# Performance work log

Hardware: AMD Instinct MI355X
Metric: run time of the kernel (lower is better)

## Reference

```python
import jax, jax.numpy as jnp
import numpy as np

NUM_USERS = 100000
NUM_ITEMS = 50000
NUM_NODES = NUM_USERS + NUM_ITEMS
EMBED_DIM = 64
NUM_LAYERS = 3
NUM_EDGES = 1200000


def setup_inputs() -> dict:
    key = jax.random.key(0)
    k1, k2 = jax.random.split(key)
    edge_index = jax.random.randint(k1, (2, NUM_EDGES), 0, NUM_NODES, dtype=jnp.int32)
    # xavier_uniform for [N, D]
    limit = float(np.sqrt(6.0 / (NUM_NODES + EMBED_DIM)))
    embedding = jax.random.uniform(k2, (NUM_NODES, EMBED_DIM), dtype=jnp.float32,
                                   minval=-limit, maxval=limit)
    return {"edge_index": edge_index, "embedding": embedding}


def reference(edge_index, embedding):
    n = embedding.shape[0]
    row, col = edge_index[0], edge_index[1]
    ones = jnp.ones((edge_index.shape[1],), dtype=embedding.dtype)
    deg_row = jax.ops.segment_sum(ones, row, num_segments=n)
    deg_col = jax.ops.segment_sum(ones, col, num_segments=n)
    # deg^-0.5 with inf (deg==0) -> 0
    inv_row = jnp.where(deg_row > 0, jax.lax.rsqrt(jnp.maximum(deg_row, 1e-30)), 0.0)
    inv_col = jnp.where(deg_col > 0, jax.lax.rsqrt(jnp.maximum(deg_col, 1e-30)), 0.0)
    norm = (inv_row[row] * inv_col[col])[:, None]  # [E, 1]

    x = embedding
    accum = x
    for _ in range(NUM_LAYERS):
        # gather source embeddings, scale by symmetric norm, scatter-add at target
        msgs = norm * x[row]                       # [E, D]
        x = jax.ops.segment_sum(msgs, col, num_segments=n)
        accum = accum + x
    final = accum / jnp.asarray(NUM_LAYERS + 1, dtype=embedding.dtype)
    return final[:NUM_USERS], final[NUM_USERS:]
```

## Files before the change

### kernel.cpp

```cpp
#include <hip/hip_runtime.h>
#include <hip/hip_fp16.h>


constexpr int NUM_USERS = 100000;
constexpr int NUM_ITEMS = 50000;
constexpr int N_NODES   = NUM_USERS + NUM_ITEMS;
constexpr int EMBED_DIM = 64;
constexpr int NUM_EDGES = 1200000;
constexpr int SHIFT = 9;
constexpr int BSZ   = 1 << SHIFT;
constexpr int NBUCK = (N_NODES + BSZ - 1) >> SHIFT;
constexpr int CAPC  = 4480;
constexpr int EPB   = 4096;
constexpr int P1_BLOCKS = (NUM_EDGES + EPB - 1) / EPB;

__global__ void __launch_bounds__(256)
pass1_bin(const int4* __restrict__ row4, const int4* __restrict__ col4,
          int* __restrict__ gcur_c, int* __restrict__ gcur_r,
          unsigned int* __restrict__ binned_c, unsigned short* __restrict__ binned_r) {
    __shared__ int hist_c[NBUCK], hist_r[NBUCK], cur_c[NBUCK], cur_r[NBUCK];
    int t = threadIdx.x;
    for (int i = t; i < NBUCK; i += 256) { hist_c[i] = 0; hist_r[i] = 0; }
    __syncthreads();
    int base4 = blockIdx.x * (EPB / 4);
    constexpr int NV = NUM_EDGES / 4;
    for (int k = 0; k < EPB / 1024; ++k) {
        int v = base4 + k * 256 + t;
        if (v < NV) {
            int4 c = col4[v];
            atomicAdd(&hist_c[c.x >> SHIFT], 1);
            atomicAdd(&hist_c[c.y >> SHIFT], 1);
            atomicAdd(&hist_c[c.z >> SHIFT], 1);
            atomicAdd(&hist_c[c.w >> SHIFT], 1);
            int4 r = row4[v];
            atomicAdd(&hist_r[r.x >> SHIFT], 1);
            atomicAdd(&hist_r[r.y >> SHIFT], 1);
            atomicAdd(&hist_r[r.z >> SHIFT], 1);
            atomicAdd(&hist_r[r.w >> SHIFT], 1);
        }
    }
    __syncthreads();
    for (int i = t; i < NBUCK; i += 256) {
        cur_c[i] = atomicAdd(&gcur_c[i], hist_c[i]);
        cur_r[i] = atomicAdd(&gcur_r[i], hist_r[i]);
    }
    __syncthreads();
    for (int k = 0; k < EPB / 1024; ++k) {
        int v = base4 + k * 256 + t;
        if (v < NV) {
            int4 c = col4[v];
            int4 r = row4[v];
            int cc[4] = {c.x, c.y, c.z, c.w};
            int rr[4] = {r.x, r.y, r.z, r.w};
#pragma unroll
            for (int q = 0; q < 4; ++q) {
                int dc = cc[q] >> SHIFT;
                int sc = atomicAdd(&cur_c[dc], 1);
                if (sc < CAPC)
                    binned_c[dc * CAPC + sc] =
                        ((unsigned)(cc[q] & (BSZ - 1)) << 18) | (unsigned)rr[q];
                int dr = rr[q] >> SHIFT;
                int sr = atomicAdd(&cur_r[dr], 1);
                if (sr < CAPC)
                    binned_r[dr * CAPC + sr] = (unsigned short)(rr[q] & (BSZ - 1));
            }
        }
    }
}

__global__ void __launch_bounds__(256)
pass2_place(const int* __restrict__ gcur_c, const int* __restrict__ gcur_r,
            const unsigned int* __restrict__ binned_c, const unsigned short* __restrict__ binned_r,
            int* __restrict__ sorted_idx, int* __restrict__ packed_pc,
            float* __restrict__ inv_col, float* __restrict__ inv_row) {
    __shared__ int hist[BSZ];
    __shared__ int partial[256];
    int t = threadIdx.x;
    hist[t] = 0; hist[t + 256] = 0;
    __syncthreads();
    int b = blockIdx.x;
    if (b < NBUCK) {
        int n = gcur_c[b]; if (n > CAPC) n = CAPC;
        const unsigned int* src = binned_c + b * CAPC;
        for (int i = t; i < n; i += 256) atomicAdd(&hist[src[i] >> 18], 1);
        int s = 0;
        for (int i = t; i < b; i += 256) s += gcur_c[i];
        partial[t] = s;
        __syncthreads();
        for (int off = 128; off > 0; off >>= 1) {
            if (t < off) partial[t] += partial[t + off];
            __syncthreads();
        }
        int bucket_base = partial[0];
        __syncthreads();
        int v0 = hist[t * 2], v1 = hist[t * 2 + 1];
        int sum = v0 + v1;
        partial[t] = sum; __syncthreads();
        for (int off = 1; off < 256; off <<= 1) {
            int tv = (t >= off) ? partial[t - off] : 0;
            __syncthreads();
            partial[t] += tv;
            __syncthreads();
        }
        int excl = partial[t] - sum;
        int o0 = excl, o1 = excl + v0;
        hist[t * 2] = o0; hist[t * 2 + 1] = o1;
        int c0 = (b << SHIFT) | (t * 2);
        if (c0 < N_NODES) {
            packed_pc[c0] = ((bucket_base + o0) << 7) | v0;
            inv_col[c0] = (v0 > 0) ? rsqrtf((float)v0) : 0.0f;
        }
        int c1 = c0 + 1;
        if (c1 < N_NODES) {
            packed_pc[c1] = ((bucket_base + o1) << 7) | v1;
            inv_col[c1] = (v1 > 0) ? rsqrtf((float)v1) : 0.0f;
        }
        __syncthreads();
        for (int i = t; i < n; i += 256) {
            unsigned int w = src[i];
            int lc = w >> 18;
            int r  = (int)(w & 0x3FFFFu);
            int slot = atomicAdd(&hist[lc], 1);
            sorted_idx[bucket_base + slot] = r;
        }
    } else {
        int bb = b - NBUCK;
        int n = gcur_r[bb]; if (n > CAPC) n = CAPC;
        const unsigned short* src = binned_r + bb * CAPC;
        for (int i = t; i < n; i += 256) atomicAdd(&hist[src[i]], 1);
        __syncthreads();
        int c0 = (bb << SHIFT) | (t * 2);
        int v0 = hist[t * 2], v1 = hist[t * 2 + 1];
        if (c0 < N_NODES)     inv_row[c0] = (v0 > 0) ? rsqrtf((float)v0) : 0.0f;
        if (c0 + 1 < N_NODES) inv_row[c0 + 1] = (v1 > 0) ? rsqrtf((float)v1) : 0.0f;
    }
}

__global__ void init_y_kernel(const float* __restrict__ inv_row,
                              const float2* __restrict__ emb2, __half2* __restrict__ y0) {
    int i = blockIdx.x * blockDim.x + threadIdx.x;
    if (i < N_NODES * (EMBED_DIM / 2)) {
        float w = inv_row[i >> 5];
        float2 e = emb2[i];
        y0[i] = __floats2half2_rn(w * e.x, w * e.y);
    }
}

__global__ void __launch_bounds__(256, 8)
layer_kernel(const int* __restrict__ packed_pc,
             const int* __restrict__ sorted_idx,
             const float* __restrict__ inv_row,
             const float* __restrict__ inv_col,
             const __half2* __restrict__ y_src,
             __half2* __restrict__ y_dst,
             float2* __restrict__ out2,
             const float2* __restrict__ emb2,
             int mode) {
    int wid  = (blockIdx.x * blockDim.x + threadIdx.x) >> 6;
    int lane = threadIdx.x & 63;
    if (wid >= N_NODES) return;
    int d2 = lane & 31;
    int eh = lane >> 5;
    int packed = packed_pc[wid];
    int cnt = packed & 127;
    int ptr = packed >> 7;
    int lidx = (cnt > 0) ? (ptr + ((lane < cnt) ? lane : 0)) : 0;
    int idx = sorted_idx[lidx];

    float ax0 = 0.0f, ay0 = 0.0f, ax1 = 0.0f, ay1 = 0.0f;
    int j = 0;
    for (; j + 4 <= cnt; j += 4) {
        int sA = __shfl(idx, j + eh);
        int sB = __shfl(idx, j + 2 + eh);
        float2 vA = __half22float2(y_src[sA * 32 + d2]);
        float2 vB = __half22float2(y_src[sB * 32 + d2]);
        ax0 += vA.x; ay0 += vA.y;
        ax1 += vB.x; ay1 += vB.y;
    }
    for (; j < cnt; j += 2) {
        int jj = j + eh;
        int sA = __shfl(idx, (jj < cnt) ? jj : 0);
        float2 vA = __half22float2(y_src[sA * 32 + d2]);
        if (jj < cnt) { ax0 += vA.x; ay0 += vA.y; }
    }
    float sx = ax0 + ax1;
    float sy = ay0 + ay1;
    sx += __shfl_xor(sx, 32);
    sy += __shfl_xor(sy, 32);

    float invc = inv_col[wid];
    float vx = sx * invc, vy = sy * invc;

    if (lane < 32) {
        int oi2 = wid * 32 + d2;
        if (mode == 0) {
            float w = inv_row[wid];
            y_dst[oi2] = __floats2half2_rn(w * vx, w * vy);
            float2 e = emb2[oi2];
            out2[oi2] = make_float2(e.x + vx, e.y + vy);
        } else if (mode == 1) {
            float w = inv_row[wid];
            y_dst[oi2] = __floats2half2_rn(w * vx, w * vy);
            float2 o = out2[oi2];
            out2[oi2] = make_float2(o.x + vx, o.y + vy);
        } else {
            float2 o = out2[oi2];
            out2[oi2] = make_float2((o.x + vx) * 0.25f, (o.y + vy) * 0.25f);
        }
    }
}

extern "C" void kernel_launch(void* const* d_in, const int* in_sizes, int n_in,
                              void* d_out, int out_size, void* d_ws, size_t ws_size,
                              hipStream_t stream) {
    const int*   edge_index = (const int*)d_in[0];
    const float* embedding  = (const float*)d_in[1];
    const int* row = edge_index;
    const int* col = edge_index + NUM_EDGES;
    float* out = (float*)d_out;

    char* ws = (char*)d_ws;
    auto align_up = [](size_t v) { return (v + 255) & ~size_t(255); };
    size_t off = 0;
    int* gcur_c     = (int*)(ws + off); off = align_up(off + sizeof(int) * NBUCK);
    int* gcur_r     = (int*)(ws + off); off = align_up(off + sizeof(int) * NBUCK);
    size_t cursor_bytes = off;
    int* packed_pc  = (int*)(ws + off); off = align_up(off + sizeof(int) * N_NODES);
    float* inv_row  = (float*)(ws + off); off = align_up(off + sizeof(float) * N_NODES);
    float* inv_col  = (float*)(ws + off); off = align_up(off + sizeof(float) * N_NODES);
    int* sorted_idx = (int*)(ws + off); off = align_up(off + sizeof(int) * NUM_EDGES);
    __half2* ya     = (__half2*)(ws + off); off = align_up(off + sizeof(__half2) * N_NODES * 32);
    __half2* yb     = (__half2*)(ws + off); off = align_up(off + sizeof(__half2) * N_NODES * 32);
    unsigned int*   binned_c = (unsigned int*)yb;
    unsigned short* binned_r = (unsigned short*)((char*)yb + align_up(sizeof(unsigned int) * NBUCK * CAPC));

    hipMemsetAsync(gcur_c, 0, cursor_bytes, stream);
    pass1_bin<<<P1_BLOCKS, 256, 0, stream>>>((const int4*)row, (const int4*)col,
                                             gcur_c, gcur_r, binned_c, binned_r);
    pass2_place<<<2 * NBUCK, 256, 0, stream>>>(gcur_c, gcur_r, binned_c, binned_r,
                                               sorted_idx, packed_pc, inv_col, inv_row);
    {
        int n2 = N_NODES * 32;
        int threads = 256, blocks = (n2 + threads - 1) / threads;
        init_y_kernel<<<blocks, threads, 0, stream>>>(inv_row, (const float2*)embedding, ya);
    }
    {
        int threads = 256;
        int blocks = (N_NODES * 64 + threads - 1) / threads;
        layer_kernel<<<blocks, threads, 0, stream>>>(packed_pc, sorted_idx, inv_row, inv_col,
                                                     ya, yb, (float2*)out,
                                                     (const float2*)embedding, 0);
        layer_kernel<<<blocks, threads, 0, stream>>>(packed_pc, sorted_idx, inv_row, inv_col,
                                                     yb, ya, (float2*)out,
                                                     (const float2*)embedding, 1);
        layer_kernel<<<blocks, threads, 0, stream>>>(packed_pc, sorted_idx, inv_row, inv_col,
                                                     ya, yb , (float2*)out,
                                                     (const float2*)embedding, 2);
    }
}
```

Baseline: 309.9 us.

## Gather eight neighbor rows per wave with 16-byte loads and split epilogue lanes

The layer kernel now has each wave cover eight edges at once, with 8 lanes each reading a 16-byte int4 slice of a half-precision row, instead of two edges with 4-byte loads. Partial sums are combined with three xor shuffles, and the epilogue is split so one lane group writes the half output and another prefetches and updates the float accumulator with float4 accesses. Pass1 binning also uses four times more blocks with one int4 per thread, for more parallelism. The change trades more shuffle reduction work and extra registers for fewer, wider memory transactions and better latency hiding on the random gathers.

```diff
diff --git a/kernel.cpp b/kernel.cpp
--- a/kernel.cpp
+++ b/kernel.cpp
@@ -11,7 +11,7 @@
 constexpr int BSZ   = 1 << SHIFT;
 constexpr int NBUCK = (N_NODES + BSZ - 1) >> SHIFT;
 constexpr int CAPC  = 4480;
-constexpr int EPB   = 4096;
+constexpr int EPB   = 1024;
 constexpr int P1_BLOCKS = (NUM_EDGES + EPB - 1) / EPB;
 
 __global__ void __launch_bounds__(256)
@@ -24,8 +24,8 @@
     __syncthreads();
     int base4 = blockIdx.x * (EPB / 4);
     constexpr int NV = NUM_EDGES / 4;
-    for (int k = 0; k < EPB / 1024; ++k) {
-        int v = base4 + k * 256 + t;
+    {
+        int v = base4 + t;
         if (v < NV) {
             int4 c = col4[v];
             atomicAdd(&hist_c[c.x >> SHIFT], 1);
@@ -45,8 +45,8 @@
         cur_r[i] = atomicAdd(&gcur_r[i], hist_r[i]);
     }
     __syncthreads();
-    for (int k = 0; k < EPB / 1024; ++k) {
-        int v = base4 + k * 256 + t;
+    {
+        int v = base4 + t;
         if (v < NV) {
             int4 c = col4[v];
             int4 r = row4[v];
@@ -151,62 +151,79 @@
              const int* __restrict__ sorted_idx,
              const float* __restrict__ inv_row,
              const float* __restrict__ inv_col,
-             const __half2* __restrict__ y_src,
-             __half2* __restrict__ y_dst,
-             float2* __restrict__ out2,
-             const float2* __restrict__ emb2,
+             const int4* __restrict__ y_src,
+             int4* __restrict__ y_dst,
+             float4* __restrict__ out4,
+             const float4* __restrict__ emb4,
              int mode) {
     int wid  = (blockIdx.x * blockDim.x + threadIdx.x) >> 6;
     int lane = threadIdx.x & 63;
     if (wid >= N_NODES) return;
-    int d2 = lane & 31;
-    int eh = lane >> 5;
+    int d4 = lane & 7;
+    int e  = lane >> 3;
     int packed = packed_pc[wid];
     int cnt = packed & 127;
     int ptr = packed >> 7;
     int lidx = (cnt > 0) ? (ptr + ((lane < cnt) ? lane : 0)) : 0;
     int idx = sorted_idx[lidx];
 
-    float ax0 = 0.0f, ay0 = 0.0f, ax1 = 0.0f, ay1 = 0.0f;
-    int j = 0;
-    for (; j + 4 <= cnt; j += 4) {
-        int sA = __shfl(idx, j + eh);
-        int sB = __shfl(idx, j + 2 + eh);
-        float2 vA = __half22float2(y_src[sA * 32 + d2]);
-        float2 vB = __half22float2(y_src[sB * 32 + d2]);
-        ax0 += vA.x; ay0 += vA.y;
-        ax1 += vB.x; ay1 += vB.y;
-    }
-    for (; j < cnt; j += 2) {
-        int jj = j + eh;
-        int sA = __shfl(idx, (jj < cnt) ? jj : 0);
-        float2 vA = __half22float2(y_src[sA * 32 + d2]);
-        if (jj < cnt) { ax0 += vA.x; ay0 += vA.y; }
-    }
-    float sx = ax0 + ax1;
-    float sy = ay0 + ay1;
-    sx += __shfl_xor(sx, 32);
-    sy += __shfl_xor(sy, 32);
-
+    int obase = wid * 16 + d4 * 2;
+    float4 o0, o1;
+    if (e == 1) {
+        const float4* src = (mode == 0) ? emb4 : (const float4*)out4;
+        o0 = src[obase];
+        o1 = src[obase + 1];
+    }
+
+    float f[8] = {0.f, 0.f, 0.f, 0.f, 0.f, 0.f, 0.f, 0.f};
+    for (int j = 0; j < cnt; j += 8) {
+        int s = __shfl(idx, j + e);
+        int4 v = y_src[s * 8 + d4];
+        if (j + e < cnt) {
+            float2 a0 = __half22float2(*reinterpret_cast<const __half2*>(&v.x));
+            float2 a1 = __half22float2(*reinterpret_cast<const __half2*>(&v.y));
+            float2 a2 = __half22float2(*reinterpret_cast<const __half2*>(&v.z));
+            float2 a3 = __half22float2(*reinterpret_cast<const __half2*>(&v.w));
+            f[0] += a0.x; f[1] += a0.y; f[2] += a1.x; f[3] += a1.y;
+            f[4] += a2.x; f[5] += a2.y; f[6] += a3.x; f[7] += a3.y;
+        }
+    }
+#pragma unroll
+    for (int k = 0; k < 8; ++k) {
+        f[k] += __shfl_xor(f[k], 8);
+        f[k] += __shfl_xor(f[k], 16);
+        f[k] += __shfl_xor(f[k], 32);
+    }
     float invc = inv_col[wid];
-    float vx = sx * invc, vy = sy * invc;
-
-    if (lane < 32) {
-        int oi2 = wid * 32 + d2;
-        if (mode == 0) {
+#pragma unroll
+    for (int k = 0; k < 8; ++k) f[k] *= invc;
+
+    if (mode != 2) {
+        if (e == 0) {
             float w = inv_row[wid];
-            y_dst[oi2] = __floats2half2_rn(w * vx, w * vy);
-            float2 e = emb2[oi2];
-            out2[oi2] = make_float2(e.x + vx, e.y + vy);
-        } else if (mode == 1) {
-            float w = inv_row[wid];
-            y_dst[oi2] = __floats2half2_rn(w * vx, w * vy);
-            float2 o = out2[oi2];
-            out2[oi2] = make_float2(o.x + vx, o.y + vy);
-        } else {
-            float2 o = out2[oi2];
-            out2[oi2] = make_float2((o.x + vx) * 0.25f, (o.y + vy) * 0.25f);
-        }
+            __half2 p0 = __floats2half2_rn(w * f[0], w * f[1]);
+            __half2 p1 = __floats2half2_rn(w * f[2], w * f[3]);
+            __half2 p2 = __floats2half2_rn(w * f[4], w * f[5]);
+            __half2 p3 = __floats2half2_rn(w * f[6], w * f[7]);
+            int4 st;
+            st.x = *reinterpret_cast<int*>(&p0);
+            st.y = *reinterpret_cast<int*>(&p1);
+            st.z = *reinterpret_cast<int*>(&p2);
+            st.w = *reinterpret_cast<int*>(&p3);
+            y_dst[wid * 8 + d4] = st;
+        } else if (e == 1) {
+            o0.x += f[0]; o0.y += f[1]; o0.z += f[2]; o0.w += f[3];
+            o1.x += f[4]; o1.y += f[5]; o1.z += f[6]; o1.w += f[7];
+            out4[obase]     = o0;
+            out4[obase + 1] = o1;
+        }
+    } else if (e == 1) {
+        o0.x = (o0.x + f[0]) * 0.25f; o0.y = (o0.y + f[1]) * 0.25f;
+        o0.z = (o0.z + f[2]) * 0.25f; o0.w = (o0.w + f[3]) * 0.25f;
+        o1.x = (o1.x + f[4]) * 0.25f; o1.y = (o1.y + f[5]) * 0.25f;
+        o1.z = (o1.z + f[6]) * 0.25f; o1.w = (o1.w + f[7]) * 0.25f;
+        out4[obase]     = o0;
+        out4[obase + 1] = o1;
     }
 }
 
@@ -248,13 +265,13 @@
         int threads = 256;
         int blocks = (N_NODES * 64 + threads - 1) / threads;
         layer_kernel<<<blocks, threads, 0, stream>>>(packed_pc, sorted_idx, inv_row, inv_col,
-                                                     ya, yb, (float2*)out,
-                                                     (const float2*)embedding, 0);
+                                                     (const int4*)ya, (int4*)yb, (float4*)out,
+                                                     (const float4*)embedding, 0);
         layer_kernel<<<blocks, threads, 0, stream>>>(packed_pc, sorted_idx, inv_row, inv_col,
-                                                     yb, ya, (float2*)out,
-                                                     (const float2*)embedding, 1);
+                                                     (const int4*)yb, (int4*)ya, (float4*)out,
+                                                     (const float4*)embedding, 1);
         layer_kernel<<<blocks, threads, 0, stream>>>(packed_pc, sorted_idx, inv_row, inv_col,
-                                                     ya, yb , (float2*)out,
-                                                     (const float2*)embedding, 2);
-    }
-}
+                                                     (const int4*)ya, (int4*)yb , (float4*)out,
+                                                     (const float4*)embedding, 2);
+    }
+}
```

New measurement: 313.2 us. No clear change (+1.1%).
